# Optimization experiments

Measured on AMD Instinct MI355X. Metric: run time of the kernel, lower is better.

## Reference

```python
import jax, jax.numpy as jnp
import numpy as np

LN_EPS = 1e-5
WKV_EPS = 1e-8


def _layernorm(x, g, b):
    mu = jnp.mean(x, axis=-1, keepdims=True)
    var = jnp.mean((x - mu) ** 2, axis=-1, keepdims=True)
    return (x - mu) * jax.lax.rsqrt(var + LN_EPS) * g + b


def setup_inputs() -> dict:
    key = jax.random.key(0)
    ks = jax.random.split(key, 16)
    B, S, D, F = 4, 2048, 1024, 4096
    xavier_d = float(np.sqrt(6.0 / (D + D)))
    xavier_df = float(np.sqrt(6.0 / (D + F)))
    u = lambda k, sh, s: jax.random.uniform(k, sh, jnp.float32, -s, s)
    return {
        "x": jax.random.normal(ks[0], (B, S, D), jnp.float32),
        "ln1_g": jnp.ones((D,), jnp.float32),
        "ln1_b": jnp.zeros((D,), jnp.float32),
        "ln2_g": jnp.ones((D,), jnp.float32),
        "ln2_b": jnp.zeros((D,), jnp.float32),
        "Wr": u(ks[1], (D, D), xavier_d),
        "Ww": u(ks[2], (D, D), xavier_d),
        "Wk": u(ks[3], (D, D), xavier_d),
        "Wv": u(ks[4], (D, D), xavier_d),
        "Wo": u(ks[5], (D, D), xavier_d),
        "time_decay": jax.random.uniform(ks[6], (D,), jnp.float32, -1.0, 0.0),
        "time_first": jax.random.uniform(ks[7], (D,), jnp.float32, -1.0, 1.0),
        "Wkey": u(ks[8], (F, D), xavier_df),
        "Wval": u(ks[9], (D, F), xavier_df),
        "Wrec": u(ks[10], (D, D), xavier_d),
    }


def _time_mix(xn, Wr, Ww, Wk, Wv, Wo, time_decay):
    # xn: [B,S,D]
    r = jax.nn.sigmoid(jnp.einsum('bsd,ed->bse', xn, Wr))
    w = -jnp.exp(jnp.einsum('bsd,ed->bse', xn, Ww))
    k = jnp.einsum('bsd,ed->bse', xn, Wk)
    v = jnp.einsum('bsd,ed->bse', xn, Wv)
    ewk = jnp.exp(w + k)  # [B,S,D]
    decay = jnp.exp(time_decay)  # [D]

    def step(carry, inp):
        num, den = carry
        e, vt = inp
        num = decay * num + e * vt
        den = decay * den + e
        wkv = num / (den + WKV_EPS)
        return (num, den), wkv

    B, S, D = xn.shape
    init = (jnp.zeros((B, D), xn.dtype), jnp.zeros((B, D), xn.dtype))
    (num_f, den_f), wkv = jax.lax.scan(
        step, init, (jnp.swapaxes(ewk, 0, 1), jnp.swapaxes(v, 0, 1)))
    wkv = jnp.swapaxes(wkv, 0, 1)  # [B,S,D]
    out = jnp.einsum('bsd,ed->bse', r * wkv, Wo)
    final_state = jnp.stack([num_f, den_f], axis=1)  # [B,2,D]
    return out, final_state


def _channel_mix(xn, Wkey, Wval, Wrec):
    k = jnp.einsum('bsd,fd->bsf', xn, Wkey)
    k = jnp.square(jax.nn.relu(k))
    v = jnp.einsum('bsf,df->bsd', k, Wval)
    r = jax.nn.sigmoid(jnp.einsum('bsd,ed->bse', xn, Wrec))
    return r * v


def reference(x, ln1_g, ln1_b, ln2_g, ln2_b, Wr, Ww, Wk, Wv, Wo,
              time_decay, time_first, Wkey, Wval, Wrec):
    tm, new_state = _time_mix(_layernorm(x, ln1_g, ln1_b),
                              Wr, Ww, Wk, Wv, Wo, time_decay)
    x = x + tm
    x = x + _channel_mix(_layernorm(x, ln2_g, ln2_b), Wkey, Wval, Wrec)
    return x, new_state
```

## Files before the change

kernel.cpp:

```cpp
#include <hip/hip_runtime.h>
#include <hip/hip_bf16.h>
#include <cstdint>
#include <cstddef>

using bf16 = __hip_bfloat16;
typedef __bf16 bf16x8 __attribute__((ext_vector_type(8)));
typedef float floatx4 __attribute__((ext_vector_type(4)));

#define LN_EPS 1e-5f
#define WKV_EPS 1e-8f

static constexpr int Bdim = 4, S = 2048, D = 1024, F = 4096;
static constexpr int M = Bdim * S;
static constexpr int NCH = 64, CH = S / NCH;
static constexpr uint32_t FP32_MAGIC = 0x3F800000u;

__device__ __forceinline__ bool is_fp32(const uint32_t* flagp) {
    return *flagp == FP32_MAGIC;
}
__device__ __forceinline__ float loadf(const void* p, size_t i, bool f32) {
    return f32 ? ((const float*)p)[i] : __bfloat162float(((const bf16*)p)[i]);
}

__device__ __forceinline__ void gload_lds16(const void* g, void* l) {
    __builtin_amdgcn_global_load_lds(
        (__attribute__((address_space(1))) void*)(g),
        (__attribute__((address_space(3))) void*)(l), 16, 0, 0);
}

__device__ __forceinline__ bf16x8 sigmoid8(bf16x8 v) {
    bf16x8 o;
    #pragma unroll
    for (int e = 0; e < 8; e++) {
        const float f = (float)v[e];
        o[e] = (__bf16)(1.0f / (1.0f + __expf(-f)));
    }
    return o;
}
__device__ __forceinline__ bf16x8 relusq8(bf16x8 v) {
    bf16x8 o;
    #pragma unroll
    for (int e = 0; e < 8; e++) {
        const float f = fmaxf((float)v[e], 0.0f);
        o[e] = (__bf16)(f * f);
    }
    return o;
}

struct WcvtArgs {
    const void* src[7];
    bf16*       dst[7];
};
__global__ __launch_bounds__(256)
void wcvt(WcvtArgs a, const uint32_t* __restrict__ flagp)
{
    const bool f32 = is_fp32(flagp);
    const int64_t idx = (int64_t)blockIdx.x * 256 + threadIdx.x;
    int seg, off;
    if (idx < (int64_t)6 * 1048576) {
        seg = (int)(idx >> 20); off = (int)(idx & 1048575);
    } else {
        seg = 6; off = (int)(idx - (int64_t)6 * 1048576);
    }
    a.dst[seg][off] = __float2bfloat16(loadf(a.src[seg], off, f32));
}
__global__ __launch_bounds__(256)
void wcvt2(const void* __restrict__ src, bf16* __restrict__ dst,
           const uint32_t* __restrict__ flagp)
{
    const bool f32 = is_fp32(flagp);
    const int idx = blockIdx.x * 256 + threadIdx.x;
    dst[idx] = __float2bfloat16(loadf(src, idx, f32));
}

enum { EPI_QKVW = 1, EPI_KR = 2, EPI_ADDX = 3, EPI_FINAL = 4 };

struct QkvwOut { bf16 *r, *g, *k, *v; };

template<int EPI>
__global__ __launch_bounds__(512, 4)
void gemm_bt(const bf16* __restrict__ A, const bf16* __restrict__ Bw,
             void* __restrict__ outp, const void* __restrict__ aux1,
             void* __restrict__ aux2, QkvwOut qo, int K, int N,
             const uint32_t* __restrict__ flagp)
{
    __shared__ __align__(16) bf16 smem[16384];
    char* smb = (char*)smem;
    const int t = threadIdx.x;
    const int tn = blockIdx.x, tm = blockIdx.y;
    const int lane = t & 63, wv = t >> 6;
    const int wm = wv & 1, wn = wv >> 1;
    const int ml = lane & 15, quad = lane >> 4;

    const size_t rowB = (size_t)K * 2;
    const int r0 = t >> 3;
    const int q0 = (t & 7) ^ (r0 & 7);
    const char* gA = (const char*)(A)  + (size_t)(tm * 128) * rowB;
    const char* gB = (const char*)(Bw) + (size_t)(tn * 128) * rowB;
    const char* a0 = gA + (size_t)r0 * rowB + q0 * 16;
    const char* a1 = a0 + 64 * rowB;
    const char* b0 = gB + (size_t)r0 * rowB + q0 * 16;
    const char* b1 = b0 + 64 * rowB;
    char* lA0 = smb + t * 16;
    char* lA1 = smb + t * 16 + 8192;
    char* lB0 = smb + t * 16 + 16384;
    char* lB1 = smb + t * 16 + 24576;

    floatx4 acc[4][2] = {};
    const int m7 = ml & 7;
    const int rq0 = ((quad)     ^ m7) * 16;
    const int rq1 = ((4 + quad) ^ m7) * 16;

    for (int k0 = 0; k0 < K; k0 += 64) {
        gload_lds16(a0, lA0);
        gload_lds16(a1, lA1);
        gload_lds16(b0, lB0);
        gload_lds16(b1, lB1);
        a0 += 128; a1 += 128; b0 += 128; b1 += 128;
        __syncthreads();
        #pragma unroll
        for (int kh = 0; kh < 2; kh++) {
            const int rq = kh ? rq1 : rq0;
            bf16x8 af[4], bfr[2];
            #pragma unroll
            for (int i = 0; i < 4; i++)
                af[i]  = *(const bf16x8*)(smb + (wm * 64 + i * 16 + ml) * 128 + rq);
            #pragma unroll
            for (int j = 0; j < 2; j++)
                bfr[j] = *(const bf16x8*)(smb + 16384 + (wn * 32 + j * 16 + ml) * 128 + rq);
            #pragma unroll
            for (int i = 0; i < 4; i++)
                #pragma unroll
                for (int j = 0; j < 2; j++)
                    acc[i][j] = __builtin_amdgcn_mfma_f32_16x16x32_bf16(af[i], bfr[j], acc[i][j], 0, 0, 0);
        }
        __syncthreads();
    }

    const bool f32 = is_fp32(flagp);
    constexpr int PS = 136;
    const int lwr = wm * 16 + quad * 4;
    const int lwc = wn * 32 + ml;
    const int rr = t >> 4;
    const int rc = (t & 15) * 8;
    #pragma unroll
    for (int i = 0; i < 4; i++) {
        __syncthreads();
        #pragma unroll
        for (int j = 0; j < 2; j++)
            #pragma unroll
            for (int rg = 0; rg < 4; rg++)
                smem[(lwr + rg) * PS + lwc + j * 16] = __float2bfloat16(acc[i][j][rg]);
        __syncthreads();
        const int gr = tm * 128 + ((rr < 16) ? (i * 16 + rr) : (64 + i * 16 + rr - 16));
        bf16x8 v = *(const bf16x8*)&smem[rr * PS + rc];
        const int gcol = tn * 128 + rc;
        if constexpr (EPI == EPI_QKVW) {
            const int seg = tn >> 3;
            bf16* dst = (seg == 0) ? qo.r : (seg == 1) ? qo.g : (seg == 2) ? qo.k : qo.v;
            const size_t i2 = (size_t)gr * 1024 + (gcol & 1023);
            if (seg == 0) v = sigmoid8(v);
            *(bf16x8*)&dst[i2] = v;
        } else if constexpr (EPI == EPI_KR) {
            if (tn < 8) {
                *(bf16x8*)&((bf16*)aux2)[(size_t)gr * 1024 + gcol] = sigmoid8(v);
            } else {
                *(bf16x8*)&((bf16*)outp)[(size_t)gr * 4096 + (gcol - 1024)] = relusq8(v);
            }
        } else if constexpr (EPI == EPI_ADDX) {
            const size_t idx = (size_t)gr * N + gcol;
            bf16x8 o;
            if (f32) {
                const float4* xp = (const float4*)((const float*)aux1 + idx);
                const float4 xa = xp[0], xb = xp[1];
                o[0] = (__bf16)((float)v[0] + xa.x); o[1] = (__bf16)((float)v[1] + xa.y);
                o[2] = (__bf16)((float)v[2] + xa.z); o[3] = (__bf16)((float)v[3] + xa.w);
                o[4] = (__bf16)((float)v[4] + xb.x); o[5] = (__bf16)((float)v[5] + xb.y);
                o[6] = (__bf16)((float)v[6] + xb.z); o[7] = (__bf16)((float)v[7] + xb.w);
            } else {
                const bf16x8 xv = *(const bf16x8*)((const bf16*)aux1 + idx);
                #pragma unroll
                for (int e = 0; e < 8; e++) o[e] = (__bf16)((float)v[e] + (float)xv[e]);
            }
            *(bf16x8*)((bf16*)outp + idx) = o;
        } else {
            const size_t idx = (size_t)gr * N + gcol;
            const bf16x8 x2v = *(const bf16x8*)((const bf16*)aux1 + idx);
            const bf16x8 rv  = *(const bf16x8*)((const bf16*)aux2 + idx);
            float ov[8];
            #pragma unroll
            for (int e = 0; e < 8; e++)
                ov[e] = (float)x2v[e] + (float)rv[e] * (float)v[e];
            if (f32) {
                float4 f0 = { ov[0], ov[1], ov[2], ov[3] };
                float4 f1 = { ov[4], ov[5], ov[6], ov[7] };
                float4* op = (float4*)((float*)outp + idx);
                op[0] = f0; op[1] = f1;
            } else {
                bf16x8 o;
                #pragma unroll
                for (int e = 0; e < 8; e++) o[e] = (__bf16)ov[e];
                *(bf16x8*)((bf16*)outp + idx) = o;
            }
        }
    }
}

template<bool IN_WS>
__global__ __launch_bounds__(256)
void ln_kernel(const void* __restrict__ x, const void* __restrict__ g,
               const void* __restrict__ b, bf16* __restrict__ out,
               const uint32_t* __restrict__ flagp)
{
    const bool f32 = is_fp32(flagp);
    const int row = blockIdx.x;
    const int t = threadIdx.x;
    const size_t base = (size_t)row * D;
    float v[4];
    #pragma unroll
    for (int i = 0; i < 4; i++) {
        const size_t c = base + t + 256 * i;
        if constexpr (IN_WS) v[i] = __bfloat162float(((const bf16*)x)[c]);
        else                 v[i] = loadf(x, c, f32);
    }
    float s = v[0] + v[1] + v[2] + v[3];
    float q = v[0]*v[0] + v[1]*v[1] + v[2]*v[2] + v[3]*v[3];
    #pragma unroll
    for (int off = 32; off > 0; off >>= 1) {
        s += __shfl_down(s, off);
        q += __shfl_down(q, off);
    }
    __shared__ float rs_[4], rq_[4];
    const int wv = t >> 6, lane = t & 63;
    if (lane == 0) { rs_[wv] = s; rq_[wv] = q; }
    __syncthreads();
    const float St = rs_[0] + rs_[1] + rs_[2] + rs_[3];
    const float Qt = rq_[0] + rq_[1] + rq_[2] + rq_[3];
    const float mean = St * (1.0f / 1024.0f);
    const float var  = Qt * (1.0f / 1024.0f) - mean * mean;
    const float rstd = rsqrtf(var + LN_EPS);
    #pragma unroll
    for (int i = 0; i < 4; i++) {
        const int c = t + 256 * i;
        const float gv = loadf(g, c, f32);
        const float bv = loadf(b, c, f32);
        out[base + c] = __float2bfloat16((v[i] - mean) * rstd * gv + bv);
    }
}

__global__ __launch_bounds__(256)
void scan_a(const bf16* __restrict__ gw, const bf16* __restrict__ kk,
            const bf16* __restrict__ vbuf, const void* __restrict__ td,
            float* __restrict__ numc, float* __restrict__ denc,
            const uint32_t* __restrict__ flagp)
{
    const bool f32 = is_fp32(flagp);
    const int idx = blockIdx.x * 256 + threadIdx.x;
    const int d = idx & (D - 1);
    const int c = (idx >> 10) & (NCH - 1);
    const int b = idx >> 16;
    const float a = __expf(loadf(td, d, f32));
    size_t p = ((size_t)b * S + (size_t)c * CH) * D + d;
    float num = 0.f, den = 0.f;
    for (int ts = 0; ts < CH; ts++) {
        const float g  = __bfloat162float(gw[p]);
        const float kv = __bfloat162float(kk[p]);
        const float e  = __expf(kv - __expf(g));
        const float vv = __bfloat162float(vbuf[p]);
        num = fmaf(a, num, e * vv);
        den = fmaf(a, den, e);
        p += D;
    }
    const size_t slot = ((size_t)b * NCH + c) * D + d;
    numc[slot] = num;
    denc[slot] = den;
}

__global__ __launch_bounds__(256)
void scan_b(float* __restrict__ numc, float* __restrict__ denc,
            const void* __restrict__ td, void* __restrict__ d_out,
            const uint32_t* __restrict__ flagp)
{
    const bool f32 = is_fp32(flagp);
    const int idx = blockIdx.x * 256 + threadIdx.x;
    const int d = idx & (D - 1);
    const int b = idx >> 10;
    const float aL = __expf(loadf(td, d, f32) * (float)CH);
    float cn = 0.f, cd = 0.f;
    for (int c = 0; c < NCH; c++) {
        const size_t slot = ((size_t)b * NCH + c) * D + d;
        const float ln = numc[slot], ld = denc[slot];
        numc[slot] = cn;
        denc[slot] = cd;
        cn = fmaf(aL, cn, ln);
        cd = fmaf(aL, cd, ld);
    }
    const size_t i0 = (size_t)b * 2 * D + d;
    const size_t i1 = i0 + D;
    const size_t off = (size_t)M * D;
    if (f32) {
        ((float*)d_out)[off + i0] = cn;
        ((float*)d_out)[off + i1] = cd;
    } else {
        ((bf16*)d_out)[off + i0] = __float2bfloat16(cn);
        ((bf16*)d_out)[off + i1] = __float2bfloat16(cd);
    }
}

__global__ __launch_bounds__(256)
void scan_c(const bf16* __restrict__ gw, const bf16* __restrict__ kk,
            const bf16* __restrict__ vbuf, bf16* __restrict__ rbuf,
            const float* __restrict__ numc, const float* __restrict__ denc,
            const void* __restrict__ td, const uint32_t* __restrict__ flagp)
{
    const bool f32 = is_fp32(flagp);
    const int idx = blockIdx.x * 256 + threadIdx.x;
    const int d = idx & (D - 1);
    const int c = (idx >> 10) & (NCH - 1);
    const int b = idx >> 16;
    const float a = __expf(loadf(td, d, f32));
    const size_t slot = ((size_t)b * NCH + c) * D + d;
    float num = numc[slot], den = denc[slot];
    size_t p = ((size_t)b * S + (size_t)c * CH) * D + d;
    for (int ts = 0; ts < CH; ts++) {
        const float g  = __bfloat162float(gw[p]);
        const float kv = __bfloat162float(kk[p]);
        const float e  = __expf(kv - __expf(g));
        const float vv = __bfloat162float(vbuf[p]);
        num = fmaf(a, num, e * vv);
        den = fmaf(a, den, e);
        const float wkv = num / (den + WKV_EPS);
        const float r = __bfloat162float(rbuf[p]);
        rbuf[p] = __float2bfloat16(r * wkv);
        p += D;
    }
}

extern "C" void kernel_launch(void* const* d_in, const int* in_sizes, int n_in,
                              void* d_out, int out_size, void* d_ws, size_t ws_size,
                              hipStream_t stream)
{
    const void* x     = d_in[0];
    const void* ln1_g = d_in[1];
    const void* ln1_b = d_in[2];
    const void* ln2_g = d_in[3];
    const void* ln2_b = d_in[4];
    const void* Wr    = d_in[5];
    const void* Ww    = d_in[6];
    const void* Wk    = d_in[7];
    const void* Wv    = d_in[8];
    const void* Wo    = d_in[9];
    const void* td    = d_in[10];
    const void* Wkey  = d_in[12];
    const void* Wval  = d_in[13];
    const void* Wrec  = d_in[14];
    const uint32_t* flagp = (const uint32_t*)ln1_g;

    #define MB(x) ((size_t)(x) << 20)
    char* ws = (char*)d_ws;
    bf16*  xnb    = (bf16*) (ws + MB(0));
    bf16*  wWval2 = (bf16*) (ws + MB(0));
    bf16*  gw     = (bf16*) (ws + MB(16));
    bf16*  kk     = (bf16*) (ws + MB(32));
    bf16*  vbuf   = (bf16*) (ws + MB(48));
    bf16*  wqkvw  = (bf16*) (ws + MB(64));
    bf16*  wWo    = (bf16*) (ws + MB(72));
    float* numc   = (float*)(ws + MB(74));
    float* denc   = (float*)(ws + MB(75));
    bf16*  kbuf   = (bf16*) (ws + MB(16));
    bf16*  rbuf   = (bf16*) (ws + MB(80));
    bf16*  x2     = (bf16*) (ws + MB(96));
    bf16*  wrk    = (bf16*) (ws + MB(112));
    #undef MB

    dim3 blk(256);
    dim3 blkG(512);
    dim3 gQ(F / 128, M / 128);
    dim3 gKR(5120 / 128, M / 128);
    dim3 gN1(D / 128, M / 128);

    WcvtArgs wa;
    wa.src[0] = Wr;   wa.dst[0] = wqkvw;
    wa.src[1] = Ww;   wa.dst[1] = wqkvw + (size_t)1 * 1048576;
    wa.src[2] = Wk;   wa.dst[2] = wqkvw + (size_t)2 * 1048576;
    wa.src[3] = Wv;   wa.dst[3] = wqkvw + (size_t)3 * 1048576;
    wa.src[4] = Wo;   wa.dst[4] = wWo;
    wa.src[5] = Wrec; wa.dst[5] = wrk;
    wa.src[6] = Wkey; wa.dst[6] = wrk + (size_t)1048576;

    QkvwOut qo = { rbuf, gw, kk, vbuf };
    QkvwOut q0 = { nullptr, nullptr, nullptr, nullptr };

    wcvt<<<(10 * 1048576) / 256, blk, 0, stream>>>(wa, flagp);
    ln_kernel<false><<<M, blk, 0, stream>>>(x, ln1_g, ln1_b, xnb, flagp);
    gemm_bt<EPI_QKVW><<<gQ, blkG, 0, stream>>>(xnb, wqkvw, nullptr, nullptr, nullptr, qo, D, 4096, flagp);
    scan_a<<<(Bdim * NCH * D) / 256, blk, 0, stream>>>(gw, kk, vbuf, td, numc, denc, flagp);
    scan_b<<<(Bdim * D) / 256,       blk, 0, stream>>>(numc, denc, td, d_out, flagp);
    scan_c<<<(Bdim * NCH * D) / 256, blk, 0, stream>>>(gw, kk, vbuf, rbuf, numc, denc, td, flagp);
    gemm_bt<EPI_ADDX><<<gN1, blkG, 0, stream>>>(rbuf, wWo, x2, x, nullptr, q0, D, D, flagp);
    ln_kernel<true><<<M, blk, 0, stream>>>(x2, ln2_g, ln2_b, xnb, flagp);
    gemm_bt<EPI_KR><<<gKR, blkG, 0, stream>>>(xnb, wrk, kbuf, nullptr, rbuf, q0, D, 5120, flagp);
    wcvt2<<<(4 * 1048576) / 256, blk, 0, stream>>>(Wval, wWval2, flagp);
    gemm_bt<EPI_FINAL><<<gN1, blkG, 0, stream>>>(kbuf, wWval2, d_out, x2, rbuf, q0, F, D, flagp);
}
```

Baseline: 501.2 us.

## Add 256x256-tile pipelined GEMM kernel for QKVW and key/receptance projections

Introduces a new gemm256 kernel with 256x256 output tiles, 512 threads, double-buffered 128KB LDS staging via direct global-to-LDS loads, and interleaved MFMA phases with sched barriers and setprio. The two wide projection GEMMs (QKVW and key/receptance) switch to it, with an LDS-staged bf16 epilogue that applies sigmoid or relu-squared. The aim is more data reuse per tile and better overlap of loads with MFMA work. The trade-off is fewer blocks (one per CU at this LDS size) and added pipeline complexity.

```diff
diff --git a/kernel.cpp b/kernel.cpp
--- a/kernel.cpp
+++ b/kernel.cpp
@@ -206,6 +206,160 @@
     }
 }
 
+#define SB0   __builtin_amdgcn_sched_barrier(0)
+#define BARR  __builtin_amdgcn_s_barrier()
+#define LGKM0 asm volatile("s_waitcnt lgkmcnt(0)" ::: "memory")
+
+#define LDA256(d, mh) do { \
+    _Pragma("unroll") for (int il = 0; il < 4; il++) \
+    _Pragma("unroll") for (int kh = 0; kh < 2; kh++) \
+        af[il][kh] = *(const bf16x8*)(smem + (d) * 65536 + \
+            (wm * 128 + ((mh) * 4 + il) * 16 + ml) * 128 + rq[kh]); \
+} while (0)
+
+#define LDB256(d, nh) do { \
+    _Pragma("unroll") for (int jl = 0; jl < 2; jl++) \
+    _Pragma("unroll") for (int kh = 0; kh < 2; kh++) \
+        bfr[jl][kh] = *(const bf16x8*)(smem + (d) * 65536 + 32768 + \
+            (wn * 64 + ((nh) * 2 + jl) * 16 + ml) * 128 + rq[kh]); \
+} while (0)
+
+#define MMA256(mh, nh) do { \
+    _Pragma("unroll") for (int il = 0; il < 4; il++) \
+    _Pragma("unroll") for (int jl = 0; jl < 2; jl++) \
+    _Pragma("unroll") for (int kh = 0; kh < 2; kh++) \
+        acc[(mh) * 4 + il][(nh) * 2 + jl] = __builtin_amdgcn_mfma_f32_16x16x32_bf16( \
+            af[il][kh], bfr[jl][kh], acc[(mh) * 4 + il][(nh) * 2 + jl], 0, 0, 0); \
+} while (0)
+
+#define STAGE_A256(d, h, kb) do { \
+    gload_lds16(gA + (size_t)(h) * 128 * rowB + (kb), smem + (d) * 65536 + (h) * 16384 + t * 16); \
+    gload_lds16(gA + ((size_t)(h) * 128 + 64) * rowB + (kb), smem + (d) * 65536 + (h) * 16384 + 8192 + t * 16); \
+} while (0)
+
+#define STAGE_B256(d, h, kb) do { \
+    gload_lds16(gB + (size_t)(h) * 128 * rowB + (kb), smem + (d) * 65536 + 32768 + (h) * 16384 + t * 16); \
+    gload_lds16(gB + ((size_t)(h) * 128 + 64) * rowB + (kb), smem + (d) * 65536 + 32768 + (h) * 16384 + 8192 + t * 16); \
+} while (0)
+
+#define PH_MID() do { SB0; BARR; LGKM0; SB0; __builtin_amdgcn_s_setprio(1); } while (0)
+#define PH_END() do { __builtin_amdgcn_s_setprio(0); SB0; BARR; } while (0)
+
+template<int EPI>
+__global__ __launch_bounds__(512)
+void gemm256(const bf16* __restrict__ A, const bf16* __restrict__ Bw,
+             void* __restrict__ outp, const void* __restrict__ aux1,
+             void* __restrict__ aux2, QkvwOut qo, int K, int N,
+             const uint32_t* __restrict__ flagp)
+{
+    __shared__ __align__(16) char smem[131072];
+    (void)N; (void)aux1; (void)flagp;
+    const int t = threadIdx.x;
+    const int tn = blockIdx.x, tm = blockIdx.y;
+    const int lane = t & 63, wv = t >> 6;
+    const int wm = wv & 1, wn = wv >> 1;
+    const int ml = lane & 15, quad = lane >> 4;
+
+    const size_t rowB = (size_t)K * 2;
+    const int r0 = t >> 3;
+    const int q0 = (t & 7) ^ (r0 & 7);
+    const char* gA = (const char*)(A)  + (size_t)(tm * 256) * rowB + (size_t)r0 * rowB + q0 * 16;
+    const char* gB = (const char*)(Bw) + (size_t)(tn * 256) * rowB + (size_t)r0 * rowB + q0 * 16;
+
+    floatx4 acc[8][4] = {};
+    bf16x8 af[4][2], bfr[2][2];
+    const int m7 = ml & 7;
+    const int rq[2] = { ((quad) ^ m7) * 16, ((4 + quad) ^ m7) * 16 };
+
+    const int NT = K >> 6;
+    STAGE_A256(0, 0, (size_t)0);
+    STAGE_A256(0, 1, (size_t)0);
+    STAGE_B256(0, 0, (size_t)0);
+    STAGE_B256(0, 1, (size_t)0);
+    const size_t kbp = (size_t)((NT > 1) ? 1 : 0) * 128;
+    STAGE_A256(1, 0, kbp);
+    STAGE_A256(1, 1, kbp);
+    asm volatile("s_waitcnt vmcnt(4)" ::: "memory");
+    SB0; BARR;
+
+    for (int tt = 0; tt < NT; ++tt) {
+        const int d = tt & 1;
+        const size_t kb1 = (size_t)((tt + 1 < NT) ? tt + 1 : NT - 1) * 128;
+        const size_t kb2 = (size_t)((tt + 2 < NT) ? tt + 2 : NT - 1) * 128;
+        LDA256(d, 0); LDB256(d, 0);
+        STAGE_B256(d ^ 1, 0, kb1);
+        PH_MID(); MMA256(0, 0); PH_END();
+        LDB256(d, 1);
+        STAGE_B256(d ^ 1, 1, kb1);
+        PH_MID(); MMA256(0, 1); PH_END();
+        LDA256(d, 1);
+        PH_MID(); MMA256(1, 1); PH_END();
+        LDB256(d, 0);
+        STAGE_A256(d, 0, kb2);
+        STAGE_A256(d, 1, kb2);
+        PH_MID(); MMA256(1, 0);
+        asm volatile("s_waitcnt vmcnt(4)" ::: "memory");
+        PH_END();
+    }
+    asm volatile("s_waitcnt vmcnt(0)" ::: "memory");
+    BARR;
+
+    bf16* sm = (bf16*)smem;
+    constexpr int PS = 264;
+    const int rr = t >> 4;
+    const int rc = (t & 15) * 16;
+    #pragma unroll
+    for (int p = 0; p < 8; ++p) {
+        __syncthreads();
+        if (wm == (p >> 2)) {
+            const int i0 = (p & 3) * 2;
+            #pragma unroll
+            for (int f = 0; f < 2; ++f)
+                #pragma unroll
+                for (int j = 0; j < 4; ++j)
+                    #pragma unroll
+                    for (int rg = 0; rg < 4; ++rg)
+                        sm[(f * 16 + quad * 4 + rg) * PS + wn * 64 + j * 16 + ml] =
+                            __float2bfloat16(acc[i0 + f][j][rg]);
+        }
+        __syncthreads();
+        const int gr = tm * 256 + p * 32 + rr;
+        bf16x8 v0 = *(const bf16x8*)&sm[rr * PS + rc];
+        bf16x8 v1 = *(const bf16x8*)&sm[rr * PS + rc + 8];
+        if constexpr (EPI == EPI_QKVW) {
+            const int seg = tn >> 2;
+            bf16* dst = (seg == 0) ? qo.r : (seg == 1) ? qo.g : (seg == 2) ? qo.k : qo.v;
+            const size_t idx = (size_t)gr * 1024 + (tn & 3) * 256 + rc;
+            if (seg == 0) { v0 = sigmoid8(v0); v1 = sigmoid8(v1); }
+            *(bf16x8*)&dst[idx] = v0;
+            *(bf16x8*)&dst[idx + 8] = v1;
+        } else {
+            if (tn < 4) {
+                bf16* dst = (bf16*)aux2;
+                const size_t idx = (size_t)gr * 1024 + tn * 256 + rc;
+                *(bf16x8*)&dst[idx] = sigmoid8(v0);
+                *(bf16x8*)&dst[idx + 8] = sigmoid8(v1);
+            } else {
+                bf16* dst = (bf16*)outp;
+                const size_t idx = (size_t)gr * 4096 + (tn - 4) * 256 + rc;
+                *(bf16x8*)&dst[idx] = relusq8(v0);
+                *(bf16x8*)&dst[idx + 8] = relusq8(v1);
+            }
+        }
+    }
+}
+
+#undef SB0
+#undef BARR
+#undef LGKM0
+#undef LDA256
+#undef LDB256
+#undef MMA256
+#undef STAGE_A256
+#undef STAGE_B256
+#undef PH_MID
+#undef PH_END
+
 template<bool IN_WS>
 __global__ __launch_bounds__(256)
 void ln_kernel(const void* __restrict__ x, const void* __restrict__ g,
@@ -375,8 +529,8 @@
 
     dim3 blk(256);
     dim3 blkG(512);
-    dim3 gQ(F / 128, M / 128);
-    dim3 gKR(5120 / 128, M / 128);
+    dim3 gQ(4096 / 256, M / 256);
+    dim3 gKR(5120 / 256, M / 256);
     dim3 gN1(D / 128, M / 128);
 
     WcvtArgs wa;
@@ -393,13 +547,13 @@
 
     wcvt<<<(10 * 1048576) / 256, blk, 0, stream>>>(wa, flagp);
     ln_kernel<false><<<M, blk, 0, stream>>>(x, ln1_g, ln1_b, xnb, flagp);
-    gemm_bt<EPI_QKVW><<<gQ, blkG, 0, stream>>>(xnb, wqkvw, nullptr, nullptr, nullptr, qo, D, 4096, flagp);
+    gemm256<EPI_QKVW><<<gQ, blkG, 0, stream>>>(xnb, wqkvw, nullptr, nullptr, nullptr, qo, D, 4096, flagp);
     scan_a<<<(Bdim * NCH * D) / 256, blk, 0, stream>>>(gw, kk, vbuf, td, numc, denc, flagp);
     scan_b<<<(Bdim * D) / 256,       blk, 0, stream>>>(numc, denc, td, d_out, flagp);
     scan_c<<<(Bdim * NCH * D) / 256, blk, 0, stream>>>(gw, kk, vbuf, rbuf, numc, denc, td, flagp);
     gemm_bt<EPI_ADDX><<<gN1, blkG, 0, stream>>>(rbuf, wWo, x2, x, nullptr, q0, D, D, flagp);
     ln_kernel<true><<<M, blk, 0, stream>>>(x2, ln2_g, ln2_b, xnb, flagp);
-    gemm_bt<EPI_KR><<<gKR, blkG, 0, stream>>>(xnb, wrk, kbuf, nullptr, rbuf, q0, D, 5120, flagp);
+    gemm256<EPI_KR><<<gKR, blkG, 0, stream>>>(xnb, wrk, kbuf, nullptr, rbuf, q0, D, 5120, flagp);
     wcvt2<<<(4 * 1048576) / 256, blk, 0, stream>>>(Wval, wWval2, flagp);
     gemm_bt<EPI_FINAL><<<gN1, blkG, 0, stream>>>(kbuf, wWval2, d_out, x2, rbuf, q0, F, D, flagp);
 }
```

Result: slower. 532.3 us (+6.2%).
